# Optimization experiments

Measured on AMD Instinct MI355X. Metric: run time of the kernel, lower is better.

Reference implementation:

```python
import jax, jax.numpy as jnp
import numpy as np

IN_DIMS = 4
DEPTH = 4
C = IN_DIMS + 1                     # channels after time augmentation
SIG = sum(C ** k for k in range(1, DEPTH + 1))  # 780
N, T = 64, 1024


def setup_inputs() -> dict:
    key = jax.random.key(0)
    k1, k2, k3, k4, k5 = jax.random.split(key, 5)
    batch = jax.random.normal(k1, (N, T, IN_DIMS), dtype=jnp.float32)
    s_c = 1.0 / np.sqrt(C)
    conv_w = jax.random.normal(k2, (C, C), dtype=jnp.float32) * s_c
    conv_b = jax.random.normal(k3, (C,), dtype=jnp.float32) * s_c
    s_l = 1.0 / np.sqrt(SIG)
    lin_w = jax.random.normal(k4, (SIG, SIG), dtype=jnp.float32) * s_l
    lin_b = jax.random.normal(k5, (SIG,), dtype=jnp.float32) * s_l
    return {"batch": batch, "conv_w": conv_w, "conv_b": conv_b,
            "lin_w": lin_w, "lin_b": lin_b}


def _stream_signature(path):
    """Streamed path signature with zero basepoint.

    path: (n, t, C). Returns (n, t, SIG) where entry t is the signature of
    the piecewise-linear path (0, path[0], ..., path[t]) truncated at DEPTH,
    levels flattened in lexicographic (row-major) order like signatory.
    """
    n = path.shape[0]
    # increments; basepoint=True means first increment is path[:,0] - 0
    dx = jnp.concatenate([path[:, :1, :], path[:, 1:, :] - path[:, :-1, :]], axis=1)
    init = tuple(jnp.zeros((n, C ** k), path.dtype) for k in range(1, DEPTH + 1))

    def step(levels, d):
        # exp(d) in the truncated tensor algebra: e_k = d^{(x)k} / k!
        e = [d]
        for k in range(2, DEPTH + 1):
            e.append((jnp.einsum('na,nb->nab', e[-1], d) / k).reshape(n, -1))
        # Chen: new_k = e_k + S_k + sum_{i=1}^{k-1} S_i (x) e_{k-i}
        new = []
        for k in range(1, DEPTH + 1):
            acc = levels[k - 1] + e[k - 1]
            for i in range(1, k):
                acc = acc + jnp.einsum('na,nb->nab', levels[i - 1], e[k - i - 1]).reshape(n, -1)
            new.append(acc)
        new = tuple(new)
        return new, jnp.concatenate(new, axis=-1)

    _, ys = jax.lax.scan(step, init, jnp.swapaxes(dx, 0, 1))  # ys: (t, n, SIG)
    return jnp.swapaxes(ys, 0, 1)


def reference(batch, conv_w, conv_b, lin_w, lin_b):
    n, t, _ = batch.shape
    # time augmentation: append channel arange(1,T+1)/T
    time = (jnp.arange(1, t + 1, dtype=batch.dtype) / t)[None, :, None]
    a = jnp.concatenate([batch, jnp.broadcast_to(time, (n, t, 1))], axis=-1)  # (n,t,C)
    # kernel-size-1 conv1d == pointwise linear over channels
    b = a @ conv_w.T + conv_b                                                  # (n,t,C)
    c = _stream_signature(b)                                                   # (n,t,SIG)
    # zero out the first stream entry (torch.concat of zeros with c[:,1:,:])
    c = jnp.concatenate([jnp.zeros((n, 1, SIG), c.dtype), c[:, 1:, :]], axis=1)
    return jnp.tanh(c @ lin_w.T + lin_b)
```

## Files before the change

### kernel.cpp

```cpp
#include <hip/hip_runtime.h>
#include <math.h>

#define N_B 64
#define T_LEN 1024
#define IN_D 4
#define CH 5
#define SIG 780
#define KP 800
#define SEG_LEN 16
#define N_SEG 64
#define SC_L1 1.0f
#define SC_L2 0.25f
#define SC_L3 0.0625f
#define SC_L4 0.015625f

typedef _Float16 f16x8 __attribute__((ext_vector_type(8)));
typedef float f32x4 __attribute__((ext_vector_type(4)));

typedef __attribute__((address_space(1))) const void* as1cp;
typedef __attribute__((address_space(3))) void* as3p;

#define VMCNT(n) asm volatile("s_waitcnt vmcnt(" #n ")" ::: "memory")

__device__ __forceinline__ float fast_tanh(float x) {
  float ax = fabsf(x);
  float e = __expf(-2.0f * ax);
  float r = (1.0f - e) * __builtin_amdgcn_rcpf(1.0f + e);
  return copysignf(r, x);
}

__global__ __launch_bounds__(256) void conv_kernel(
    const float* __restrict__ batch,
    const float* __restrict__ conv_w,
    const float* __restrict__ conv_b,
    float* __restrict__ b_out) {
  int idx = blockIdx.x * blockDim.x + threadIdx.x;
  if (idx >= N_B * T_LEN) return;
  int t = idx & (T_LEN - 1);
  const float* a = batch + (size_t)idx * IN_D;
  float a0 = a[0], a1 = a[1], a2 = a[2], a3 = a[3];
  float tm = (float)(t + 1) / (float)T_LEN;
  float* o = b_out + (size_t)idx * CH;
#pragma unroll
  for (int j = 0; j < CH; ++j) {
    const float* w = conv_w + j * CH;
    float r = conv_b[j];
    r = fmaf(tm, w[4], r);
    r = fmaf(a3, w[3], r);
    r = fmaf(a2, w[2], r);
    r = fmaf(a1, w[1], r);
    r = fmaf(a0, w[0], r);
    o[j] = r;
  }
}

__global__ __launch_bounds__(320) void seg_kernel(
    const float* __restrict__ batch,
    const float* __restrict__ conv_w,
    const float* __restrict__ conv_b,
    float* __restrict__ P) {
  int s = blockIdx.x;
  int n = blockIdx.y;
  int tid = threadIdx.x;

  __shared__ float S[SIG];
  __shared__ float bc[(SEG_LEN + 1) * CH];
  __shared__ float dsh[SEG_LEN][CH];

  for (int i = tid; i < SIG; i += 320) S[i] = 0.0f;
  if (tid < (SEG_LEN + 1) * CH) {
    int r = s * SEG_LEN - 1 + tid / CH, ch = tid % CH;
    float v = 0.0f;
    if (r >= 0) {
      const float* a = batch + ((size_t)n * T_LEN + r) * IN_D;
      const float* w = conv_w + ch * CH;
      v = conv_b[ch];
      v = fmaf(a[0], w[0], v);
      v = fmaf(a[1], w[1], v);
      v = fmaf(a[2], w[2], v);
      v = fmaf(a[3], w[3], v);
      v = fmaf((float)(r + 1) * (1.0f / T_LEN), w[4], v);
    }
    bc[tid] = v;
  }
  __syncthreads();
  if (tid < SEG_LEN * CH) {
    int j = tid / CH, ch = tid % CH;
    dsh[j][ch] = bc[(j + 1) * CH + ch] - bc[j * CH + ch];
  }

  const int x0 = tid;
  const int x1 = tid + 320;
  const bool has1 = (tid < 305);
  const int a0i = x0 / 125, b0i = (x0 / 25) % 5, c0i = (x0 / 5) % 5, d0i = x0 % 5;
  const int a1i = x1 / 125, b1i = (x1 / 25) % 5, c1i = (x1 / 5) % 5, d1i = x1 % 5;
  const int s2_0 = x0 / 25, s3_0 = x0 / 5;
  const int s2_1 = x1 / 25, s3_1 = x1 / 5;
  const bool hasL3 = (tid < 125);
  const int ya = tid / 25, yb = (tid / 5) % 5, yc = tid % 5;
  const bool hasL2 = (tid < 25);
  const int za = tid / 5, zb = tid % 5;
  const bool hasL1 = (tid < CH);
  __syncthreads();

  for (int j = 0; j < SEG_LEN; ++j) {
    float n4_0, n4_1 = 0.0f, n3 = 0.0f, n2 = 0.0f, n1 = 0.0f;
    {
      float tH = fmaf(0.25f, dsh[j][a0i], S[a0i]);
      tH = fmaf((1.0f / 3.0f) * dsh[j][b0i], tH, S[5 + s2_0]);
      tH = fmaf(0.5f * dsh[j][c0i], tH, S[30 + s3_0]);
      n4_0 = fmaf(dsh[j][d0i], tH, S[155 + x0]);
    }
    if (has1) {
      float tH = fmaf(0.25f, dsh[j][a1i], S[a1i]);
      tH = fmaf((1.0f / 3.0f) * dsh[j][b1i], tH, S[5 + s2_1]);
      tH = fmaf(0.5f * dsh[j][c1i], tH, S[30 + s3_1]);
      n4_1 = fmaf(dsh[j][d1i], tH, S[155 + x1]);
    }
    if (hasL3) {
      float tH = fmaf((1.0f / 3.0f), dsh[j][ya], S[ya]);
      tH = fmaf(0.5f * dsh[j][yb], tH, S[5 + ya * 5 + yb]);
      n3 = fmaf(dsh[j][yc], tH, S[30 + tid]);
    }
    if (hasL2) {
      float tH = fmaf(0.5f, dsh[j][za], S[za]);
      n2 = fmaf(dsh[j][zb], tH, S[5 + tid]);
    }
    if (hasL1) n1 = S[tid] + dsh[j][tid];
    __syncthreads();
    S[155 + x0] = n4_0;
    if (has1) S[155 + x1] = n4_1;
    if (hasL3) S[30 + tid] = n3;
    if (hasL2) S[5 + tid] = n2;
    if (hasL1) S[tid] = n1;
    __syncthreads();
  }

  float* Pr = P + ((size_t)n * N_SEG + s) * SIG;
  for (int i = tid; i < SIG; i += 320) Pr[i] = S[i];
}

__global__ __launch_bounds__(640) void prefix_kernel(float* __restrict__ P) {
  int n = blockIdx.x;
  int tid = threadIdx.x;
  __shared__ float A[SIG];
  __shared__ float Bs[SIG];

  float* Pn = P + (size_t)n * N_SEG * SIG;
  for (int i = tid; i < SIG; i += 640) A[i] = Pn[i];
  int i0 = tid, i1 = tid + 640;
  float r0 = 0.f, r1 = 0.f;
  if (i0 < SIG) r0 = Pn[SIG + i0];
  if (i1 < SIG) r1 = Pn[SIG + i1];

  const int e4 = tid;
  const int q4a = e4 / 125, r125 = e4 % 125, r25 = e4 % 25, r5 = e4 % 5;
  const int e4d5 = e4 / 5, e4d25 = e4 / 25;
  const int e3 = tid;
  const int e3a = e3 / 25, e3r25 = e3 % 25, e3r5 = e3 % 5, e3d5 = e3 / 5;
  const int e2 = tid - 125;
  const int e1 = tid - 150;

  for (int s = 1; s < N_SEG; ++s) {
    if (i0 < SIG) Bs[i0] = r0;
    if (i1 < SIG) Bs[i1] = r1;
    __syncthreads();
    if (s + 1 < N_SEG) {
      const float* Pnx = Pn + (size_t)(s + 1) * SIG;
      if (i0 < SIG) r0 = Pnx[i0];
      if (i1 < SIG) r1 = Pnx[i1];
    }
    float v4 = 0.f, v3 = 0.f, v2 = 0.f, v1 = 0.f;
    if (tid < 625) {
      v4 = A[155 + e4] + Bs[155 + e4];
      v4 = fmaf(A[30 + e4d5], Bs[r5], v4);
      v4 = fmaf(A[5 + e4d25], Bs[5 + r25], v4);
      v4 = fmaf(A[q4a], Bs[30 + r125], v4);
    }
    if (tid < 125) {
      v3 = A[30 + e3] + Bs[30 + e3];
      v3 = fmaf(A[5 + e3d5], Bs[e3r5], v3);
      v3 = fmaf(A[e3a], Bs[5 + e3r25], v3);
    } else if (tid < 150) {
      v2 = A[5 + e2] + Bs[5 + e2];
      v2 = fmaf(A[e2 / 5], Bs[e2 % 5], v2);
    } else if (tid < 155) {
      v1 = A[e1] + Bs[e1];
    }
    __syncthreads();
    float* Po = Pn + (size_t)s * SIG;
    if (tid < 625) { A[155 + e4] = v4; Po[155 + e4] = v4; }
    if (tid < 125) { A[30 + e3] = v3; Po[30 + e3] = v3; }
    else if (tid < 150) { A[5 + e2] = v2; Po[5 + e2] = v2; }
    else if (tid < 155) { A[e1] = v1; Po[e1] = v1; }
  }
}

__global__ __launch_bounds__(320) void emit_kernel(
    const float* __restrict__ batch,
    const float* __restrict__ conv_w,
    const float* __restrict__ conv_b,
    const float* __restrict__ P,
    _Float16* __restrict__ c1,
    _Float16* __restrict__ c2) {
  int s = blockIdx.x;
  int n = blockIdx.y;
  int tid = threadIdx.x;

  __shared__ float S[SIG];
  __shared__ float bc[(SEG_LEN + 1) * CH];
  __shared__ float dsh[SEG_LEN][CH];
  __shared__ __align__(16) _Float16 row1[KP];
  __shared__ __align__(16) _Float16 row2[KP];

  if (s == 0) {
    for (int i = tid; i < SIG; i += 320) S[i] = 0.0f;
  } else {
    const float* Pr = P + ((size_t)n * N_SEG + (s - 1)) * SIG;
    for (int i = tid; i < SIG; i += 320) S[i] = Pr[i];
  }
  if (tid < (SEG_LEN + 1) * CH) {
    int r = s * SEG_LEN - 1 + tid / CH, ch = tid % CH;
    float v = 0.0f;
    if (r >= 0) {
      const float* a = batch + ((size_t)n * T_LEN + r) * IN_D;
      const float* w = conv_w + ch * CH;
      v = conv_b[ch];
      v = fmaf(a[0], w[0], v);
      v = fmaf(a[1], w[1], v);
      v = fmaf(a[2], w[2], v);
      v = fmaf(a[3], w[3], v);
      v = fmaf((float)(r + 1) * (1.0f / T_LEN), w[4], v);
    }
    bc[tid] = v;
  }
  if (tid < KP - SIG) {
    row1[SIG + tid] = (_Float16)0.0f;
    row2[SIG + tid] = (_Float16)0.0f;
  }
  __syncthreads();
  if (tid < SEG_LEN * CH) {
    int j = tid / CH, ch = tid % CH;
    dsh[j][ch] = bc[(j + 1) * CH + ch] - bc[j * CH + ch];
  }

  const int x0 = tid;
  const int x1 = tid + 320;
  const bool has1 = (tid < 305);
  const int a0i = x0 / 125, b0i = (x0 / 25) % 5, c0i = (x0 / 5) % 5, d0i = x0 % 5;
  const int a1i = x1 / 125, b1i = (x1 / 25) % 5, c1i = (x1 / 5) % 5, d1i = x1 % 5;
  const int s2_0 = x0 / 25, s3_0 = x0 / 5;
  const int s2_1 = x1 / 25, s3_1 = x1 / 5;
  const bool hasL3 = (tid < 125);
  const int ya = tid / 25, yb = (tid / 5) % 5, yc = tid % 5;
  const bool hasL2 = (tid < 25);
  const int za = tid / 5, zb = tid % 5;
  const bool hasL1 = (tid < CH);
  __syncthreads();

  for (int j = 0; j < SEG_LEN; ++j) {
    int t = s * SEG_LEN + j;
    float n4_0, n4_1 = 0.0f, n3 = 0.0f, n2 = 0.0f, n1 = 0.0f;
    {
      float tH = fmaf(0.25f, dsh[j][a0i], S[a0i]);
      tH = fmaf((1.0f / 3.0f) * dsh[j][b0i], tH, S[5 + s2_0]);
      tH = fmaf(0.5f * dsh[j][c0i], tH, S[30 + s3_0]);
      n4_0 = fmaf(dsh[j][d0i], tH, S[155 + x0]);
    }
    if (has1) {
      float tH = fmaf(0.25f, dsh[j][a1i], S[a1i]);
      tH = fmaf((1.0f / 3.0f) * dsh[j][b1i], tH, S[5 + s2_1]);
      tH = fmaf(0.5f * dsh[j][c1i], tH, S[30 + s3_1]);
      n4_1 = fmaf(dsh[j][d1i], tH, S[155 + x1]);
    }
    if (hasL3) {
      float tH = fmaf((1.0f / 3.0f), dsh[j][ya], S[ya]);
      tH = fmaf(0.5f * dsh[j][yb], tH, S[5 + ya * 5 + yb]);
      n3 = fmaf(dsh[j][yc], tH, S[30 + tid]);
    }
    if (hasL2) {
      float tH = fmaf(0.5f, dsh[j][za], S[za]);
      n2 = fmaf(dsh[j][zb], tH, S[5 + tid]);
    }
    if (hasL1) n1 = S[tid] + dsh[j][tid];
    __syncthreads();

    S[155 + x0] = n4_0;
    if (has1) S[155 + x1] = n4_1;
    if (hasL3) S[30 + tid] = n3;
    if (hasL2) S[5 + tid] = n2;
    if (hasL1) S[tid] = n1;

    float z = (t == 0) ? 0.0f : 1.0f;
    {
      float v = n4_0 * SC_L4 * z;
      _Float16 h = (_Float16)v;
      row1[155 + x0] = h; row2[155 + x0] = (_Float16)(v - (float)h);
    }
    if (has1) {
      float v = n4_1 * SC_L4 * z;
      _Float16 h = (_Float16)v;
      row1[155 + x1] = h; row2[155 + x1] = (_Float16)(v - (float)h);
    }
    if (hasL3) {
      float v = n3 * SC_L3 * z;
      _Float16 h = (_Float16)v;
      row1[30 + tid] = h; row2[30 + tid] = (_Float16)(v - (float)h);
    }
    if (hasL2) {
      float v = n2 * SC_L2 * z;
      _Float16 h = (_Float16)v;
      row1[5 + tid] = h; row2[5 + tid] = (_Float16)(v - (float)h);
    }
    if (hasL1) {
      float v = n1 * SC_L1 * z;
      _Float16 h = (_Float16)v;
      row1[tid] = h; row2[tid] = (_Float16)(v - (float)h);
    }
    __syncthreads();

    size_t base = ((size_t)n * T_LEN + t) * KP;
    if (tid < 100) {
      *(float4*)(c1 + base + tid * 8) = *(const float4*)&row1[tid * 8];
    } else if (tid < 200) {
      int c = tid - 100;
      *(float4*)(c2 + base + c * 8) = *(const float4*)&row2[c * 8];
    }
  }
}

__global__ __launch_bounds__(256) void wconv_kernel(
    const float* __restrict__ W,
    _Float16* __restrict__ w1,
    _Float16* __restrict__ w2) {
  int idx = blockIdx.x * blockDim.x + threadIdx.x;
  if (idx >= 896 * KP) return;
  int nn = idx / KP, k = idx % KP;
  float v = 0.0f;
  if (nn < SIG && k < SIG) {
    float sc = (k < 5) ? 1.0f : (k < 30) ? 4.0f : (k < 155) ? 16.0f : 64.0f;
    v = W[(size_t)nn * SIG + k] * sc;
  }
  _Float16 h = (_Float16)v;
  w1[idx] = h;
  w2[idx] = (_Float16)(v - (float)h);
}

__global__ __launch_bounds__(512, 2) void gemm_mfma(
    const _Float16* __restrict__ A1p, const _Float16* __restrict__ A2p,
    const _Float16* __restrict__ B1p, const _Float16* __restrict__ B2p,
    const float* __restrict__ bias, float* __restrict__ out) {
  __shared__ _Float16 Al[3][2][256 * 32];
  __shared__ _Float16 Bl[3][2][128 * 32];

  int tid = threadIdx.x;
  int lane = tid & 63, wid = tid >> 6;
  int wm = wid >> 1, wn = wid & 1;

  int b = blockIdx.x;
  int xcd = b & 7, sidx = b >> 3;
  int mt = (sidx / 7) * 8 + xcd;
  int nt = sidx % 7;
  int m0 = mt * 256;
  int n0 = nt * 128;

  f32x4 acc[4][4];
#pragma unroll
  for (int i = 0; i < 4; ++i)
#pragma unroll
    for (int j = 0; j < 4; ++j) acc[i][j] = (f32x4){0.f, 0.f, 0.f, 0.f};

  int sr = lane >> 2, scn = lane & 3;
  int swst = (sr ^ (sr >> 2)) & 3;
  int qg = scn ^ swst;
  int fr = lane & 15, fq = lane >> 4;
  int swf = (fr ^ (fr >> 2)) & 3;
  int fchunk = fq ^ swf;

  auto stageA = [&](int kb, int buf, int i) {
    int k0 = kb * 32;
    int linear = wid * 4 + i;
    int plane = linear >> 4, grp = linear & 15;
    size_t g = (size_t)(m0 + grp * 16 + sr) * KP + k0 + qg * 8;
    const _Float16* src = (plane ? A2p : A1p) + g;
    __builtin_amdgcn_global_load_lds((as1cp)src, (as3p)(&Al[buf][plane][grp * 512]), 16, 0, 0);
  };
  auto stageB = [&](int kb, int buf, int i) {
    int k0 = kb * 32;
    int linear = wid * 2 + i;
    int plane = linear >> 3, grp = linear & 7;
    size_t g = (size_t)(n0 + grp * 16 + sr) * KP + k0 + qg * 8;
    const _Float16* src = (plane ? B2p : B1p) + g;
    __builtin_amdgcn_global_load_lds((as1cp)src, (as3p)(&Bl[buf][plane][grp * 512]), 16, 0, 0);
  };

#pragma unroll
  for (int i = 0; i < 4; ++i) stageA(0, 0, i);
#pragma unroll
  for (int i = 0; i < 2; ++i) stageB(0, 0, i);
#pragma unroll
  for (int i = 0; i < 4; ++i) stageA(1, 1, i);
#pragma unroll
  for (int i = 0; i < 2; ++i) stageB(1, 1, i);

  f16x8 b1f[4], b2f[4];
  int cur = 0;
#pragma unroll 1
  for (int kb = 0; kb < 25; ++kb) {
    int nx = cur + 2; if (nx >= 3) nx -= 3;
    bool pf = (kb + 2 < 25);
    if (kb < 24) { VMCNT(6); } else { VMCNT(0); }
    __builtin_amdgcn_s_barrier();
    __builtin_amdgcn_sched_barrier(0);
#pragma unroll
    for (int ph = 0; ph < 2; ++ph) {
      f16x8 a1f[2], a2f[2];
      if (ph == 0) {
#pragma unroll
        for (int tn = 0; tn < 4; ++tn) {
          int off = (wn * 64 + tn * 16 + fr) * 32 + fchunk * 8;
          b1f[tn] = *(const f16x8*)&Bl[cur][0][off];
          b2f[tn] = *(const f16x8*)&Bl[cur][1][off];
        }
      }
#pragma unroll
      for (int t = 0; t < 2; ++t) {
        int tm = ph * 2 + t;
        int off = (wm * 64 + tm * 16 + fr) * 32 + fchunk * 8;
        a1f[t] = *(const f16x8*)&Al[cur][0][off];
        a2f[t] = *(const f16x8*)&Al[cur][1][off];
      }
      if (pf) {
        stageA(kb + 2, nx, ph * 2 + 0);
        stageA(kb + 2, nx, ph * 2 + 1);
        stageB(kb + 2, nx, ph);
      }
      __builtin_amdgcn_s_barrier();
      __builtin_amdgcn_sched_barrier(0);
      __builtin_amdgcn_s_setprio(1);
#pragma unroll
      for (int t = 0; t < 2; ++t) {
        int tm = ph * 2 + t;
#pragma unroll
        for (int tn = 0; tn < 4; ++tn) {
          acc[tm][tn] = __builtin_amdgcn_mfma_f32_16x16x32_f16(a1f[t], b1f[tn], acc[tm][tn], 0, 0, 0);
          acc[tm][tn] = __builtin_amdgcn_mfma_f32_16x16x32_f16(a1f[t], b2f[tn], acc[tm][tn], 0, 0, 0);
          acc[tm][tn] = __builtin_amdgcn_mfma_f32_16x16x32_f16(a2f[t], b1f[tn], acc[tm][tn], 0, 0, 0);
        }
      }
      __builtin_amdgcn_s_setprio(0);
    }
    cur = cur + 1; if (cur >= 3) cur -= 3;
  }
  __syncthreads();

  float* ep = (float*)(&Al[0][0][0]) + wid * 2112;

  float bv[4];
#pragma unroll
  for (int tn = 0; tn < 4; ++tn) {
    int nn = n0 + wn * 64 + tn * 16 + fr;
    bv[tn] = (nn < SIG) ? bias[nn] : 0.0f;
  }
#pragma unroll
  for (int h = 0; h < 2; ++h) {
#pragma unroll
    for (int tm2 = 0; tm2 < 2; ++tm2) {
      int tm = h * 2 + tm2;
#pragma unroll
      for (int tn = 0; tn < 4; ++tn) {
#pragma unroll
        for (int r = 0; r < 4; ++r) {
          int lr = tm2 * 16 + fq * 4 + r;
          int lc = tn * 16 + fr;
          ep[lr * 66 + lc] = fast_tanh(acc[tm][tn][r] + bv[tn]);
        }
      }
    }
#pragma unroll
    for (int p = 0; p < 2; ++p) {
      int lr = lane & 31;
      int ck = (lane >> 5) * 2 + p;
      int gm = m0 + wm * 64 + h * 32 + lr;
      int gc0 = n0 + wn * 64 + ck * 16;
#pragma unroll
      for (int q = 0; q < 4; ++q) {
        int col = gc0 + q * 4;
        if (col + 3 < SIG) {
          *(float4*)(out + (size_t)gm * SIG + col) =
              *(const float4*)&ep[lr * 66 + ck * 16 + q * 4];
        } else if (col < SIG) {
#pragma unroll
          for (int e = 0; e < 4; ++e) {
            int c2 = col + e;
            if (c2 < SIG) out[(size_t)gm * SIG + c2] = ep[lr * 66 + ck * 16 + q * 4 + e];
          }
        }
      }
    }
  }
}

__global__ __launch_bounds__(320) void sig_kernel_fb(
    const float* __restrict__ b_in, float* __restrict__ c_out) {
  int n = blockIdx.x;
  int tid = threadIdx.x;
  __shared__ float S[SIG];
  __shared__ float bc[64 * CH];
  __shared__ float dsh[CH];
  __shared__ float pb[CH];
  for (int i = tid; i < SIG; i += 320) S[i] = 0.0f;
  if (tid < CH) pb[tid] = 0.0f;
  const float* bn = b_in + (size_t)n * T_LEN * CH;
  float* cn = c_out + (size_t)n * T_LEN * SIG;
  const int x0 = tid, x1 = tid + 320;
  const bool has1 = (tid < 305);
  const int a0i = x0 / 125, b0i = (x0 / 25) % 5, c0i = (x0 / 5) % 5, d0i = x0 % 5;
  const int a1i = x1 / 125, b1i = (x1 / 25) % 5, c1i = (x1 / 5) % 5, d1i = x1 % 5;
  const int s2_0 = x0 / 25, s3_0 = x0 / 5, s2_1 = x1 / 25, s3_1 = x1 / 5;
  const bool hasL3 = (tid < 125);
  const int ya = tid / 25, yb = (tid / 5) % 5, yc = tid % 5;
  const bool hasL2 = (tid < 25);
  const int za = tid / 5, zb = tid % 5;
  const bool hasL1 = (tid < CH);
  for (int t = 0; t < T_LEN; ++t) {
    if ((t & 63) == 0) {
      __syncthreads();
      bc[tid] = bn[t * CH + tid];
      __syncthreads();
    }
    if (tid < CH) {
      float cur = bc[(t & 63) * CH + tid];
      dsh[tid] = cur - pb[tid];
      pb[tid] = cur;
    }
    __syncthreads();
    float n4_0, n4_1 = 0.0f, n3 = 0.0f, n2 = 0.0f, n1 = 0.0f;
    {
      float tH = fmaf(0.25f, dsh[a0i], S[a0i]);
      tH = fmaf((1.0f / 3.0f) * dsh[b0i], tH, S[5 + s2_0]);
      tH = fmaf(0.5f * dsh[c0i], tH, S[30 + s3_0]);
      n4_0 = fmaf(dsh[d0i], tH, S[155 + x0]);
    }
    if (has1) {
      float tH = fmaf(0.25f, dsh[a1i], S[a1i]);
      tH = fmaf((1.0f / 3.0f) * dsh[b1i], tH, S[5 + s2_1]);
      tH = fmaf(0.5f * dsh[c1i], tH, S[30 + s3_1]);
      n4_1 = fmaf(dsh[d1i], tH, S[155 + x1]);
    }
    if (hasL3) {
      float tH = fmaf((1.0f / 3.0f), dsh[ya], S[ya]);
      tH = fmaf(0.5f * dsh[yb], tH, S[5 + ya * 5 + yb]);
      n3 = fmaf(dsh[yc], tH, S[30 + tid]);
    }
    if (hasL2) {
      float tH = fmaf(0.5f, dsh[za], S[za]);
      n2 = fmaf(dsh[zb], tH, S[5 + tid]);
    }
    if (hasL1) n1 = S[tid] + dsh[tid];
    __syncthreads();
    S[155 + x0] = n4_0;
    if (has1) S[155 + x1] = n4_1;
    if (hasL3) S[30 + tid] = n3;
    if (hasL2) S[5 + tid] = n2;
    if (hasL1) S[tid] = n1;
    float* crow = cn + (size_t)t * SIG;
    float z = (t == 0) ? 0.0f : 1.0f;
    crow[155 + x0] = n4_0 * z;
    if (has1) crow[155 + x1] = n4_1 * z;
    if (hasL3) crow[30 + tid] = n3 * z;
    if (hasL2) crow[5 + tid] = n2 * z;
    if (hasL1) crow[tid] = n1 * z;
    __syncthreads();
  }
}

#define BM 256
#define BN 64
#define BK 16
__global__ __launch_bounds__(256) void gemm_tanh_fb(
    const float* __restrict__ Cmat, const float* __restrict__ W,
    const float* __restrict__ bias, float* __restrict__ out) {
  __shared__ float As[BK][BM + 4];
  __shared__ float Ws[BK][BN + 4];
  int tid = threadIdx.x;
  int tx = tid & 7, ty = tid >> 3;
  int m0 = blockIdx.x * BM, n0 = blockIdx.y * BN;
  float acc[8][8];
#pragma unroll
  for (int i = 0; i < 8; ++i)
#pragma unroll
    for (int j = 0; j < 8; ++j) acc[i][j] = 0.0f;
  for (int kb = 0; kb < SIG; kb += BK) {
    __syncthreads();
#pragma unroll
    for (int p = 0; p < 4; ++p) {
      int id = tid + p * 256;
      int row = id >> 2, kg = (id & 3) * 4, gk = kb + kg;
      float4 v = make_float4(0.f, 0.f, 0.f, 0.f);
      if (gk < SIG) v = *(const float4*)(Cmat + (size_t)(m0 + row) * SIG + gk);
      As[kg + 0][row] = v.x; As[kg + 1][row] = v.y;
      As[kg + 2][row] = v.z; As[kg + 3][row] = v.w;
    }
    {
      int row = tid >> 2, kg = (tid & 3) * 4, gk = kb + kg, wr = n0 + row;
      float4 v = make_float4(0.f, 0.f, 0.f, 0.f);
      if (gk < SIG && wr < SIG) v = *(const float4*)(W + (size_t)wr * SIG + gk);
      Ws[kg + 0][row] = v.x; Ws[kg + 1][row] = v.y;
      Ws[kg + 2][row] = v.z; Ws[kg + 3][row] = v.w;
    }
    __syncthreads();
#pragma unroll
    for (int k = 0; k < BK; ++k) {
      float af[8], wf[8];
      *(float4*)&af[0] = *(const float4*)&As[k][ty * 8];
      *(float4*)&af[4] = *(const float4*)&As[k][ty * 8 + 4];
      *(float4*)&wf[0] = *(const float4*)&Ws[k][tx * 8];
      *(float4*)&wf[4] = *(const float4*)&Ws[k][tx * 8 + 4];
#pragma unroll
      for (int i = 0; i < 8; ++i)
#pragma unroll
        for (int j = 0; j < 8; ++j) acc[i][j] = fmaf(af[i], wf[j], acc[i][j]);
    }
  }
#pragma unroll
  for (int i = 0; i < 8; ++i) {
    int m = m0 + ty * 8 + i;
    float* orow = out + (size_t)m * SIG;
#pragma unroll
    for (int jj = 0; jj < 8; jj += 4) {
      int col = n0 + tx * 8 + jj;
      if (col < SIG) {
        float4 r;
        r.x = tanhf(acc[i][jj + 0] + bias[col + 0]);
        r.y = tanhf(acc[i][jj + 1] + bias[col + 1]);
        r.z = tanhf(acc[i][jj + 2] + bias[col + 2]);
        r.w = tanhf(acc[i][jj + 3] + bias[col + 3]);
        *(float4*)(orow + col) = r;
      }
    }
  }
}

extern "C" void kernel_launch(void* const* d_in, const int* in_sizes, int n_in,
                              void* d_out, int out_size, void* d_ws, size_t ws_size,
                              hipStream_t stream) {
  const float* batch = (const float*)d_in[0];
  const float* conv_w = (const float*)d_in[1];
  const float* conv_b = (const float*)d_in[2];
  const float* lin_w = (const float*)d_in[3];
  const float* lin_b = (const float*)d_in[4];
  float* out = (float*)d_out;

  const size_t plane_elems = (size_t)N_B * T_LEN * KP;
  const size_t wplane_elems = (size_t)896 * KP;
  const size_t P_elems = (size_t)N_B * N_SEG * SIG;
  const size_t bp_elems = (size_t)N_B * T_LEN * CH;
  const size_t need_big = 2 * plane_elems * sizeof(_Float16) +
                          2 * wplane_elems * sizeof(_Float16) +
                          P_elems * sizeof(float);

  if (ws_size >= need_big) {
    _Float16* c1 = (_Float16*)d_ws;
    _Float16* c2 = c1 + plane_elems;
    _Float16* w1 = c2 + plane_elems;
    _Float16* w2 = w1 + wplane_elems;
    float* P = (float*)(w2 + wplane_elems);

    wconv_kernel<<<dim3((896 * KP + 255) / 256), dim3(256), 0, stream>>>(
        lin_w, w1, w2);
    seg_kernel<<<dim3(N_SEG, N_B), dim3(320), 0, stream>>>(batch, conv_w, conv_b, P);
    prefix_kernel<<<dim3(N_B), dim3(640), 0, stream>>>(P);
    emit_kernel<<<dim3(N_SEG, N_B), dim3(320), 0, stream>>>(
        batch, conv_w, conv_b, P, c1, c2);
    gemm_mfma<<<dim3(1792), dim3(512), 0, stream>>>(c1, c2, w1, w2, lin_b, out);
  } else {
    float* b_path = (float*)d_ws;
    float* c_sig = (float*)d_ws + bp_elems;
    conv_kernel<<<dim3((N_B * T_LEN + 255) / 256), dim3(256), 0, stream>>>(
        batch, conv_w, conv_b, b_path);
    sig_kernel_fb<<<dim3(N_B), dim3(320), 0, stream>>>(b_path, c_sig);
    gemm_tanh_fb<<<dim3((N_B * T_LEN) / BM, (SIG + BN - 1) / BN), dim3(256), 0, stream>>>(
        c_sig, lin_w, lin_b, out);
  }
}
```

Baseline: 662.0 us.

## Load B fragments directly into registers and use 4-stage LDS ring for A

The GEMM no longer stages the B (weight) tile through LDS. Each wave loads its B fragments straight from global memory into registers, double-buffered across k-steps, while A uses a 4-deep LDS ring with a single barrier per k-step instead of two phases. This is meant to cut LDS traffic and barrier count and to give more prefetch depth for A. In exchange it uses more VGPRs and issues uncoalesced 16-byte global reads for B, with no LDS-based sharing of B across waves.

Measured after the change: 777.8 us. 1.17x slower.

```diff
diff --git a/kernel.cpp b/kernel.cpp
--- a/kernel.cpp
+++ b/kernel.cpp
@@ -350,8 +350,7 @@
     const _Float16* __restrict__ A1p, const _Float16* __restrict__ A2p,
     const _Float16* __restrict__ B1p, const _Float16* __restrict__ B2p,
     const float* __restrict__ bias, float* __restrict__ out) {
-  __shared__ _Float16 Al[3][2][256 * 32];
-  __shared__ _Float16 Bl[3][2][128 * 32];
+  __shared__ _Float16 Al[4][2][256 * 32];
 
   int tid = threadIdx.x;
   int lane = tid & 63, wid = tid >> 6;
@@ -385,73 +384,78 @@
     const _Float16* src = (plane ? A2p : A1p) + g;
     __builtin_amdgcn_global_load_lds((as1cp)src, (as3p)(&Al[buf][plane][grp * 512]), 16, 0, 0);
   };
-  auto stageB = [&](int kb, int buf, int i) {
-    int k0 = kb * 32;
-    int linear = wid * 2 + i;
-    int plane = linear >> 3, grp = linear & 7;
-    size_t g = (size_t)(n0 + grp * 16 + sr) * KP + k0 + qg * 8;
-    const _Float16* src = (plane ? B2p : B1p) + g;
-    __builtin_amdgcn_global_load_lds((as1cp)src, (as3p)(&Bl[buf][plane][grp * 512]), 16, 0, 0);
-  };
-
+
+  const _Float16* bb1[4];
+  const _Float16* bb2[4];
+#pragma unroll
+  for (int tn = 0; tn < 4; ++tn) {
+    size_t off = (size_t)(n0 + wn * 64 + tn * 16 + fr) * KP + fq * 8;
+    bb1[tn] = B1p + off;
+    bb2[tn] = B2p + off;
+  }
+
+  f16x8 bX1[4], bX2[4], bY1[4], bY2[4];
+
+#pragma unroll
+  for (int tn = 0; tn < 4; ++tn) {
+    bX1[tn] = *(const f16x8*)(bb1[tn]);
+    bX2[tn] = *(const f16x8*)(bb2[tn]);
+  }
+  __builtin_amdgcn_sched_barrier(0);
 #pragma unroll
   for (int i = 0; i < 4; ++i) stageA(0, 0, i);
-#pragma unroll
-  for (int i = 0; i < 2; ++i) stageB(0, 0, i);
+  __builtin_amdgcn_sched_barrier(0);
 #pragma unroll
   for (int i = 0; i < 4; ++i) stageA(1, 1, i);
-#pragma unroll
-  for (int i = 0; i < 2; ++i) stageB(1, 1, i);
-
-  f16x8 b1f[4], b2f[4];
-  int cur = 0;
+
+#define BODY(kb, bufi, C1, C2, N1, N2, MODE)                                          \
+  {                                                                                   \
+    if ((MODE) == 2) { VMCNT(0); } else { VMCNT(4); }                                 \
+    __builtin_amdgcn_s_barrier();                                                     \
+    __builtin_amdgcn_sched_barrier(0);                                                \
+    f16x8 a1f[4], a2f[4];                                                             \
+    _Pragma("unroll") for (int tm = 0; tm < 4; ++tm) {                                \
+      int off = (wm * 64 + tm * 16 + fr) * 32 + fchunk * 8;                           \
+      a1f[tm] = *(const f16x8*)&Al[bufi][0][off];                                     \
+      a2f[tm] = *(const f16x8*)&Al[bufi][1][off];                                     \
+    }                                                                                 \
+    if ((MODE) < 2) {                                                                 \
+      _Pragma("unroll") for (int tn = 0; tn < 4; ++tn) {                              \
+        N1[tn] = *(const f16x8*)(bb1[tn] + ((kb) + 1) * 32);                          \
+        N2[tn] = *(const f16x8*)(bb2[tn] + ((kb) + 1) * 32);                          \
+      }                                                                               \
+    }                                                                                 \
+    __builtin_amdgcn_sched_barrier(0);                                                \
+    if ((MODE) == 0) {                                                                \
+      _Pragma("unroll") for (int i = 0; i < 4; ++i) stageA((kb) + 2, ((kb) + 2) & 3, i); \
+    }                                                                                 \
+    __builtin_amdgcn_sched_barrier(0);                                                \
+    __builtin_amdgcn_s_setprio(1);                                                    \
+    _Pragma("unroll") for (int tm = 0; tm < 4; ++tm) {                                \
+      _Pragma("unroll") for (int tn = 0; tn < 4; ++tn) {                              \
+        acc[tm][tn] = __builtin_amdgcn_mfma_f32_16x16x32_f16(a1f[tm], C1[tn], acc[tm][tn], 0, 0, 0); \
+        acc[tm][tn] = __builtin_amdgcn_mfma_f32_16x16x32_f16(a1f[tm], C2[tn], acc[tm][tn], 0, 0, 0); \
+        acc[tm][tn] = __builtin_amdgcn_mfma_f32_16x16x32_f16(a2f[tm], C1[tn], acc[tm][tn], 0, 0, 0); \
+      }                                                                               \
+    }                                                                                 \
+    __builtin_amdgcn_s_setprio(0);                                                    \
+  }
+
 #pragma unroll 1
-  for (int kb = 0; kb < 25; ++kb) {
-    int nx = cur + 2; if (nx >= 3) nx -= 3;
-    bool pf = (kb + 2 < 25);
-    if (kb < 24) { VMCNT(6); } else { VMCNT(0); }
-    __builtin_amdgcn_s_barrier();
-    __builtin_amdgcn_sched_barrier(0);
-#pragma unroll
-    for (int ph = 0; ph < 2; ++ph) {
-      f16x8 a1f[2], a2f[2];
-      if (ph == 0) {
-#pragma unroll
-        for (int tn = 0; tn < 4; ++tn) {
-          int off = (wn * 64 + tn * 16 + fr) * 32 + fchunk * 8;
-          b1f[tn] = *(const f16x8*)&Bl[cur][0][off];
-          b2f[tn] = *(const f16x8*)&Bl[cur][1][off];
-        }
-      }
-#pragma unroll
-      for (int t = 0; t < 2; ++t) {
-        int tm = ph * 2 + t;
-        int off = (wm * 64 + tm * 16 + fr) * 32 + fchunk * 8;
-        a1f[t] = *(const f16x8*)&Al[cur][0][off];
-        a2f[t] = *(const f16x8*)&Al[cur][1][off];
-      }
-      if (pf) {
-        stageA(kb + 2, nx, ph * 2 + 0);
-        stageA(kb + 2, nx, ph * 2 + 1);
-        stageB(kb + 2, nx, ph);
-      }
-      __builtin_amdgcn_s_barrier();
-      __builtin_amdgcn_sched_barrier(0);
-      __builtin_amdgcn_s_setprio(1);
-#pragma unroll
-      for (int t = 0; t < 2; ++t) {
-        int tm = ph * 2 + t;
-#pragma unroll
-        for (int tn = 0; tn < 4; ++tn) {
-          acc[tm][tn] = __builtin_amdgcn_mfma_f32_16x16x32_f16(a1f[t], b1f[tn], acc[tm][tn], 0, 0, 0);
-          acc[tm][tn] = __builtin_amdgcn_mfma_f32_16x16x32_f16(a1f[t], b2f[tn], acc[tm][tn], 0, 0, 0);
-          acc[tm][tn] = __builtin_amdgcn_mfma_f32_16x16x32_f16(a2f[t], b1f[tn], acc[tm][tn], 0, 0, 0);
-        }
-      }
-      __builtin_amdgcn_s_setprio(0);
-    }
-    cur = cur + 1; if (cur >= 3) cur -= 3;
-  }
+  for (int kq = 0; kq < 5; ++kq) {
+    int kb = kq * 4;
+    BODY(kb + 0, 0, bX1, bX2, bY1, bY2, 0);
+    BODY(kb + 1, 1, bY1, bY2, bX1, bX2, 0);
+    BODY(kb + 2, 2, bX1, bX2, bY1, bY2, 0);
+    BODY(kb + 3, 3, bY1, bY2, bX1, bX2, 0);
+  }
+  BODY(20, 0, bX1, bX2, bY1, bY2, 0);
+  BODY(21, 1, bY1, bY2, bX1, bX2, 0);
+  BODY(22, 2, bX1, bX2, bY1, bY2, 0);
+  BODY(23, 3, bY1, bY2, bX1, bX2, 1);
+  BODY(24, 0, bX1, bX2, bY1, bY2, 2);
+#undef BODY
+
   __syncthreads();
 
   float* ep = (float*)(&Al[0][0][0]) + wid * 2112;
```
